# Performance work log

Measured on AMD Instinct MI355X. Metric: run time of the kernel, lower is better.

Reference implementation:

```python
import jax, jax.numpy as jnp
import numpy as np

IN_F, OUT_F, GS = 4096, 4096, 128
N_GROUPS = OUT_F * IN_F // GS  # 131072
TOKENS = 8192  # batch 4 * seq 2048


def setup_inputs() -> dict:
    key = jax.random.key(0)
    k1, k2, k3 = jax.random.split(key, 3)
    x = jax.random.normal(k1, (TOKENS, IN_F), dtype=jnp.float32)
    # ternary values in {-1, 0, 1}
    ternary = jax.random.randint(k2, (OUT_F, IN_F), -1, 2, dtype=jnp.int32).astype(jnp.int8)
    # per-group positive scales (beta), like abs-mean init, clamped > 0
    scales = jax.random.uniform(k3, (N_GROUPS,), dtype=jnp.float32, minval=0.01, maxval=0.1)
    ste_gain = jnp.ones((1,), dtype=jnp.float32)
    ste_temp = jnp.ones((1,), dtype=jnp.float32)
    return {"x": x, "ternary": ternary, "scales": scales,
            "ste_gain": ste_gain, "ste_temp": ste_temp}


def reference(x, ternary, scales, ste_gain, ste_temp):
    # Dequantize: each group of GS consecutive weights (row-major over [out,in])
    # shares one scale. scale_exp has shape [OUT_F, IN_F].
    scale_exp = jnp.repeat(scales, GS).reshape(OUT_F, IN_F)
    w = ternary.astype(jnp.float32) * scale_exp  # [out, in]
    # F.linear(x, w) = x @ w.T  (ste_gain/ste_temp affect only backward)
    return jnp.dot(x, w.T)
```

## Files before the change

kernel.cpp:

```cpp
#include <hip/hip_runtime.h>

#define TOKENS 8192
#define IN_F   4096
#define OUT_F  4096

#define BM 256
#define BN 256
#define BK 64
#define NT (IN_F / BK)

typedef __attribute__((ext_vector_type(4))) float  f32x4;
typedef __attribute__((ext_vector_type(4))) int    i32x4;

typedef const __attribute__((address_space(1))) void gas_void;
typedef __attribute__((address_space(3))) void las_void;

__global__ __launch_bounds__(256) void quant_x_kernel(const float* __restrict__ x,
                                                      signed char* __restrict__ xq,
                                                      float* __restrict__ dx) {
    const int row  = blockIdx.x;
    const int tid  = threadIdx.x;
    const int lane = tid & 63;
    const int wv   = tid >> 6;
    const float* xr = x + (size_t)row * IN_F;

    float v[16];
#pragma unroll
    for (int k = 0; k < 4; ++k) {
        f32x4 t = *(const f32x4*)(xr + k * 1024 + tid * 4);
#pragma unroll
        for (int j = 0; j < 4; ++j) v[k * 4 + j] = t[j];
    }
    float m = 0.f;
#pragma unroll
    for (int j = 0; j < 16; ++j) m = fmaxf(m, fabsf(v[j]));
#pragma unroll
    for (int off = 32; off >= 1; off >>= 1) m = fmaxf(m, __shfl_xor(m, off));
    __shared__ float sm[4];
    if (lane == 0) sm[wv] = m;
    __syncthreads();
    m = fmaxf(fmaxf(sm[0], sm[1]), fmaxf(sm[2], sm[3]));

    const float inv = 127.0f / m;
    if (tid == 0) dx[row] = m * (1.0f / 127.0f);

    int* out = (int*)(xq + (size_t)row * IN_F);
#pragma unroll
    for (int k = 0; k < 4; ++k) {
        int p = 0;
#pragma unroll
        for (int j = 0; j < 4; ++j) {
            int q = (int)rintf(v[k * 4 + j] * inv);
            p |= (q & 0xff) << (8 * j);
        }
        out[k * 256 + tid] = p;
    }
}

__global__ __launch_bounds__(256) void quant_w_kernel(const int* __restrict__ tern,
                                                      const float* __restrict__ scales,
                                                      signed char* __restrict__ wq,
                                                      float* __restrict__ dw) {
    const int o0   = blockIdx.x << 4;
    const int tid  = threadIdx.x;
    const int lane = tid & 63;
    const int lr   = lane & 15;
    const int lg   = lane >> 4;
    const int kt0  = tid >> 6;

    const int o = o0 + lr;
    const float* sr = scales + o * 32;
    float smax = 0.f;
#pragma unroll
    for (int g = 0; g < 32; ++g) smax = fmaxf(smax, sr[g]);
    const float rs = 127.0f / smax;
    if (tid < 16) dw[o0 + tid] = smax * (1.0f / 127.0f);

    const int bn  = o0 >> 8;
    const int g16 = (o0 >> 4) & 15;
    signed char* outb = wq + ((size_t)((bn * 64) * 16 + g16) << 10) + lane * 16;

#pragma unroll
    for (int i = 0; i < 16; ++i) {
        const int kt = kt0 * 16 + i;
        const int c  = kt * 4 + lg;
        const int iq = (int)rintf(sr[c >> 3] * rs);
        const i32x4* tp = (const i32x4*)(tern + (size_t)o * IN_F + c * 16);
        i32x4 w4;
#pragma unroll
        for (int k = 0; k < 4; ++k) {
            i32x4 tt = tp[k];
            int p = 0;
#pragma unroll
            for (int j = 0; j < 4; ++j) p |= ((tt[j] * iq) & 0xff) << (8 * j);
            w4[k] = p;
        }
        *(i32x4*)(outb + ((size_t)(kt * 16) << 10)) = w4;
    }
}


#define QUAD(MI0, NI0, BC)                                                     \
  do {                                                                         \
    __builtin_amdgcn_s_setprio(1);                                             \
    _Pragma("unroll") for (int mi = 0; mi < 4; ++mi)                           \
      _Pragma("unroll") for (int ni = 0; ni < 2; ++ni)                         \
          acc[(MI0)+mi][(NI0)+ni] = __builtin_amdgcn_mfma_i32_16x16x64_i8(     \
              a[(MI0)+mi], BC[(NI0)+ni], acc[(MI0)+mi][(NI0)+ni], 0, 0, 0);    \
    __builtin_amdgcn_s_setprio(0);                                             \
  } while (0)

#define BODY(T, BC, BNX)                                                       \
  do {                                                                         \
    const int abase_ = ((T) % 3) * 16384;                                      \
    _Pragma("unroll") for (int mi = 0; mi < 8; ++mi)                           \
        a[mi] = *(const i32x4*)&As[abase_ + pA[mi]];                           \
    if ((T) + 1 < NT) {                                                        \
      _Pragma("unroll") for (int ni = 0; ni < 4; ++ni)                         \
          BNX[ni] = *(const i32x4*)(bF + ni * 1024 + ((T) + 1) * 16384);       \
    }                                                                          \
    if ((T) + 2 < NT) stage_tile(((T) + 2) % 3, ((T) + 2) * BK);               \
    QUAD(0, 0, BC); QUAD(0, 2, BC); QUAD(4, 0, BC); QUAD(4, 2, BC);            \
    if ((T) + 2 < NT)      asm volatile("s_waitcnt vmcnt(6)" ::: "memory");    \
    else if ((T) + 1 < NT) asm volatile("s_waitcnt vmcnt(4)" ::: "memory");    \
    __builtin_amdgcn_sched_barrier(0);                                         \
    __builtin_amdgcn_s_barrier();                                              \
    __builtin_amdgcn_sched_barrier(0);                                         \
  } while (0)

__global__ __launch_bounds__(512, 2) void gemm_i8_kernel(
        const signed char* __restrict__ A,
        const signed char* __restrict__ B,
        const float* __restrict__ dX,
        const float* __restrict__ dW,
        float* __restrict__ C) {
    __shared__ __align__(16) signed char As[3 * 16384];

    const int tid  = threadIdx.x;
    const int wave = tid >> 6;
    const int lane = tid & 63;
    const int wm   = wave >> 2;
    const int wn   = wave & 3;
    const int lg   = lane >> 4;
    const int lr   = lane & 15;

    int bid = blockIdx.x;
    bid = (bid & 7) * (512 >> 3) + (bid >> 3);
    const int bm = bid >> 4;
    const int bn = bid & 15;

    const size_t a_row0 = (size_t)bm * BM;
    const size_t b_row0 = (size_t)bn * BN;

    const int sx  = (tid & 7) ^ ((tid >> 3) & 7);
    const int s_r = ((tid >> 3) << 1) | ((sx >> 2) & 1);
    const int s_c = (sx & 3) << 4;

    auto stage_half = [&](int buf, int h, int k0) {
        const signed char* src = A + (a_row0 + h * 128 + s_r) * IN_F + k0 + s_c;
        signed char* dst = As + buf * 16384 + h * 8192 + (wave << 10);
        __builtin_amdgcn_global_load_lds((gas_void*)src, (las_void*)dst, 16, 0, 0);
    };
    auto stage_tile = [&](int buf, int k0) { stage_half(buf, 0, k0); stage_half(buf, 1, k0); };

    i32x4 acc[8][4] = {};
    i32x4 a[8], bA[4], bB[4];

    auto physoff = [&](int r, int c0) {
        return ((r >> 1) << 7) + (((((r & 1) << 6) | c0) ^ (((r >> 1) & 7) << 4)));
    };
    int pA[8];
#pragma unroll
    for (int mi = 0; mi < 8; ++mi) pA[mi] = physoff(wm * 128 + mi * 16 + lr, lg << 4);

    const signed char* bF = B + ((size_t)(bn * 64 * 16 + wn * 4) << 10) + lane * 16;

    stage_tile(0, 0); stage_tile(1, BK);
#pragma unroll
    for (int ni = 0; ni < 4; ++ni) bA[ni] = *(const i32x4*)(bF + ni * 1024);
    asm volatile("s_waitcnt vmcnt(6)" ::: "memory");
    __builtin_amdgcn_sched_barrier(0);
    __builtin_amdgcn_s_barrier();
    __builtin_amdgcn_sched_barrier(0);

    for (int tt = 0; tt < NT; tt += 2) {
        BODY(tt,     bA, bB);
        BODY(tt + 1, bB, bA);
    }

    float dwc[4];
#pragma unroll
    for (int ni = 0; ni < 4; ++ni) dwc[ni] = dW[b_row0 + wn * 64 + ni * 16 + lr];

    float* Cp = C + (a_row0 + wm * 128) * (size_t)OUT_F + b_row0 + wn * 64;
#pragma unroll
    for (int mi = 0; mi < 8; ++mi) {
#pragma unroll
        for (int j = 0; j < 4; ++j) {
            const int r = mi * 16 + lg * 4 + j;
            const float dxr = dX[a_row0 + wm * 128 + r];
#pragma unroll
            for (int ni = 0; ni < 4; ++ni)
                Cp[(size_t)r * OUT_F + ni * 16 + lr] =
                    (float)acc[mi][ni][j] * dxr * dwc[ni];
        }
    }
}

extern "C" void kernel_launch(void* const* d_in, const int* in_sizes, int n_in,
                              void* d_out, int out_size, void* d_ws, size_t ws_size,
                              hipStream_t stream) {
    const float* x      = (const float*)d_in[0];
    const int*   tern   = (const int*)d_in[1];
    const float* scales = (const float*)d_in[2];

    signed char* xq = (signed char*)d_ws;
    signed char* wq = xq + (size_t)TOKENS * IN_F;
    float*       dx = (float*)(wq + (size_t)OUT_F * IN_F);
    float*       dw = dx + TOKENS;

    quant_x_kernel<<<TOKENS, 256, 0, stream>>>(x, xq, dx);
    quant_w_kernel<<<OUT_F / 16, 256, 0, stream>>>(tern, scales, wq, dw);

    dim3 grid((TOKENS / BM) * (OUT_F / BN));
    gemm_i8_kernel<<<grid, 512, 0, stream>>>(xq, wq, dx, dw, (float*)d_out);
}
```

Measured before the change: 203.5 us.

## Pre-swizzle activations into MFMA fragment layout and load both operands directly to registers

The activation quantize kernel now handles 16 rows per block and writes int8 activations in the same fragment-tiled layout used for weights. The GEMM drops the LDS staging and the barriers and loads A and B fragments straight from global memory into double-buffered registers, and the block-to-tile mapping changes. This removes LDS traffic and synchronisation, but each wave now fetches its own A fragments from global/L2 with no sharing, and load latency is hidden only by register double buffering.

```diff
diff --git a/kernel.cpp b/kernel.cpp
--- a/kernel.cpp
+++ b/kernel.cpp
@@ -12,48 +12,51 @@
 typedef __attribute__((ext_vector_type(4))) float  f32x4;
 typedef __attribute__((ext_vector_type(4))) int    i32x4;
 
-typedef const __attribute__((address_space(1))) void gas_void;
-typedef __attribute__((address_space(3))) void las_void;
+__global__ __launch_bounds__(256) void quant_x_kernel(const float* __restrict__ x,
+                                                      signed char* __restrict__ aq,
+                                                      float* __restrict__ dx) {
+    const int g   = blockIdx.x;
+    const int tid = threadIdx.x;
+    const float* xr0 = x + (size_t)g * 16 * IN_F;
 
-__global__ __launch_bounds__(256) void quant_x_kernel(const float* __restrict__ x,
-                                                      signed char* __restrict__ xq,
-                                                      float* __restrict__ dx) {
-    const int row  = blockIdx.x;
-    const int tid  = threadIdx.x;
-    const int lane = tid & 63;
-    const int wv   = tid >> 6;
-    const float* xr = x + (size_t)row * IN_F;
+    const int r1 = tid >> 4;
+    const int c1 = tid & 15;
+    float m = 0.f;
+    const float* p = xr0 + (size_t)r1 * IN_F + c1 * 4;
+    for (int s = 0; s < 64; ++s) {
+        f32x4 v = *(const f32x4*)(p + s * 64);
+        m = fmaxf(fmaxf(fabsf(v[0]), fabsf(v[1])),
+                  fmaxf(fmaxf(fabsf(v[2]), fabsf(v[3])), m));
+    }
+#pragma unroll
+    for (int off = 1; off < 16; off <<= 1) m = fmaxf(m, __shfl_xor(m, off));
+    __shared__ float sm[16];
+    if (c1 == 0) sm[r1] = m;
+    __syncthreads();
+    if (tid < 16) dx[g * 16 + tid] = sm[tid] * (1.0f / 127.0f);
 
-    float v[16];
+    const int lane = tid & 63, w = tid >> 6;
+    const int lr = lane & 15, cg = lane >> 4;
+    const float inv = 127.0f / sm[lr];
+    const float* xp = xr0 + (size_t)lr * IN_F;
+    signed char* outb = aq + (((size_t)(w * 16) * 512 + g) << 10) + lane * 16;
+
+    for (int s = 0; s < 16; ++s) {
+        const int kt = w * 16 + s;
+        const f32x4* src = (const f32x4*)(xp + kt * 64 + cg * 16);
+        i32x4 o;
 #pragma unroll
-    for (int k = 0; k < 4; ++k) {
-        f32x4 t = *(const f32x4*)(xr + k * 1024 + tid * 4);
+        for (int k = 0; k < 4; ++k) {
+            f32x4 v = src[k];
+            int pk = 0;
 #pragma unroll
-        for (int j = 0; j < 4; ++j) v[k * 4 + j] = t[j];
-    }
-    float m = 0.f;
-#pragma unroll
-    for (int j = 0; j < 16; ++j) m = fmaxf(m, fabsf(v[j]));
-#pragma unroll
-    for (int off = 32; off >= 1; off >>= 1) m = fmaxf(m, __shfl_xor(m, off));
-    __shared__ float sm[4];
-    if (lane == 0) sm[wv] = m;
-    __syncthreads();
-    m = fmaxf(fmaxf(sm[0], sm[1]), fmaxf(sm[2], sm[3]));
-
-    const float inv = 127.0f / m;
-    if (tid == 0) dx[row] = m * (1.0f / 127.0f);
-
-    int* out = (int*)(xq + (size_t)row * IN_F);
-#pragma unroll
-    for (int k = 0; k < 4; ++k) {
-        int p = 0;
-#pragma unroll
-        for (int j = 0; j < 4; ++j) {
-            int q = (int)rintf(v[k * 4 + j] * inv);
-            p |= (q & 0xff) << (8 * j);
+            for (int j = 0; j < 4; ++j) {
+                int q = (int)rintf(v[j] * inv);
+                pk |= (q & 0xff) << (8 * j);
+            }
+            o[k] = pk;
         }
-        out[k * 256 + tid] = p;
+        *(i32x4*)(outb + ((size_t)s * 512 << 10)) = o;
     }
 }
 
@@ -90,42 +93,32 @@
 #pragma unroll
         for (int k = 0; k < 4; ++k) {
             i32x4 tt = tp[k];
-            int p = 0;
+            int pk = 0;
 #pragma unroll
-            for (int j = 0; j < 4; ++j) p |= ((tt[j] * iq) & 0xff) << (8 * j);
-            w4[k] = p;
+            for (int j = 0; j < 4; ++j) pk |= ((tt[j] * iq) & 0xff) << (8 * j);
+            w4[k] = pk;
         }
         *(i32x4*)(outb + ((size_t)(kt * 16) << 10)) = w4;
     }
 }
 
 
-#define QUAD(MI0, NI0, BC)                                                     \
+#define MFMA_ALL(AF, BF)                                                       \
   do {                                                                         \
     __builtin_amdgcn_s_setprio(1);                                             \
-    _Pragma("unroll") for (int mi = 0; mi < 4; ++mi)                           \
-      _Pragma("unroll") for (int ni = 0; ni < 2; ++ni)                         \
-          acc[(MI0)+mi][(NI0)+ni] = __builtin_amdgcn_mfma_i32_16x16x64_i8(     \
-              a[(MI0)+mi], BC[(NI0)+ni], acc[(MI0)+mi][(NI0)+ni], 0, 0, 0);    \
+    _Pragma("unroll") for (int mi = 0; mi < 8; ++mi)                           \
+      _Pragma("unroll") for (int ni = 0; ni < 4; ++ni)                         \
+          acc[mi][ni] = __builtin_amdgcn_mfma_i32_16x16x64_i8(                 \
+              AF[mi], BF[ni], acc[mi][ni], 0, 0, 0);                           \
     __builtin_amdgcn_s_setprio(0);                                             \
   } while (0)
 
-#define BODY(T, BC, BNX)                                                       \
+#define LOADF(AF, BF, T)                                                       \
   do {                                                                         \
-    const int abase_ = ((T) % 3) * 16384;                                      \
     _Pragma("unroll") for (int mi = 0; mi < 8; ++mi)                           \
-        a[mi] = *(const i32x4*)&As[abase_ + pA[mi]];                           \
-    if ((T) + 1 < NT) {                                                        \
-      _Pragma("unroll") for (int ni = 0; ni < 4; ++ni)                         \
-          BNX[ni] = *(const i32x4*)(bF + ni * 1024 + ((T) + 1) * 16384);       \
-    }                                                                          \
-    if ((T) + 2 < NT) stage_tile(((T) + 2) % 3, ((T) + 2) * BK);               \
-    QUAD(0, 0, BC); QUAD(0, 2, BC); QUAD(4, 0, BC); QUAD(4, 2, BC);            \
-    if ((T) + 2 < NT)      asm volatile("s_waitcnt vmcnt(6)" ::: "memory");    \
-    else if ((T) + 1 < NT) asm volatile("s_waitcnt vmcnt(4)" ::: "memory");    \
-    __builtin_amdgcn_sched_barrier(0);                                         \
-    __builtin_amdgcn_s_barrier();                                              \
-    __builtin_amdgcn_sched_barrier(0);                                         \
+        AF[mi] = *(const i32x4*)(aB + (((size_t)(T) * 512 + mi) << 10));       \
+    _Pragma("unroll") for (int ni = 0; ni < 4; ++ni)                           \
+        BF[ni] = *(const i32x4*)(bB + (((size_t)(T) * 16 + ni) << 10));        \
   } while (0)
 
 __global__ __launch_bounds__(512, 2) void gemm_i8_kernel(
@@ -134,8 +127,6 @@
         const float* __restrict__ dX,
         const float* __restrict__ dW,
         float* __restrict__ C) {
-    __shared__ __align__(16) signed char As[3 * 16384];
-
     const int tid  = threadIdx.x;
     const int wave = tid >> 6;
     const int lane = tid & 63;
@@ -144,48 +135,28 @@
     const int lg   = lane >> 4;
     const int lr   = lane & 15;
 
-    int bid = blockIdx.x;
-    bid = (bid & 7) * (512 >> 3) + (bid >> 3);
-    const int bm = bid >> 4;
-    const int bn = bid & 15;
+    const int bid = blockIdx.x;
+    const int bn  = ((bid & 7) << 1) | (bid >> 8);
+    const int bm  = (bid >> 3) & 31;
 
     const size_t a_row0 = (size_t)bm * BM;
     const size_t b_row0 = (size_t)bn * BN;
 
-    const int sx  = (tid & 7) ^ ((tid >> 3) & 7);
-    const int s_r = ((tid >> 3) << 1) | ((sx >> 2) & 1);
-    const int s_c = (sx & 3) << 4;
-
-    auto stage_half = [&](int buf, int h, int k0) {
-        const signed char* src = A + (a_row0 + h * 128 + s_r) * IN_F + k0 + s_c;
-        signed char* dst = As + buf * 16384 + h * 8192 + (wave << 10);
-        __builtin_amdgcn_global_load_lds((gas_void*)src, (las_void*)dst, 16, 0, 0);
-    };
-    auto stage_tile = [&](int buf, int k0) { stage_half(buf, 0, k0); stage_half(buf, 1, k0); };
+    const signed char* aB = A + (((size_t)(bm * 16 + wm * 8)) << 10) + lane * 16;
+    const signed char* bB = B + (((size_t)(bn * 64 * 16 + wn * 4)) << 10) + lane * 16;
 
     i32x4 acc[8][4] = {};
-    i32x4 a[8], bA[4], bB[4];
+    i32x4 aX[8], bX[4], aY[8], bY[4];
 
-    auto physoff = [&](int r, int c0) {
-        return ((r >> 1) << 7) + (((((r & 1) << 6) | c0) ^ (((r >> 1) & 7) << 4)));
-    };
-    int pA[8];
-#pragma unroll
-    for (int mi = 0; mi < 8; ++mi) pA[mi] = physoff(wm * 128 + mi * 16 + lr, lg << 4);
+    LOADF(aX, bX, 0);
+    LOADF(aY, bY, 1);
 
-    const signed char* bF = B + ((size_t)(bn * 64 * 16 + wn * 4) << 10) + lane * 16;
-
-    stage_tile(0, 0); stage_tile(1, BK);
-#pragma unroll
-    for (int ni = 0; ni < 4; ++ni) bA[ni] = *(const i32x4*)(bF + ni * 1024);
-    asm volatile("s_waitcnt vmcnt(6)" ::: "memory");
-    __builtin_amdgcn_sched_barrier(0);
-    __builtin_amdgcn_s_barrier();
-    __builtin_amdgcn_sched_barrier(0);
-
-    for (int tt = 0; tt < NT; tt += 2) {
-        BODY(tt,     bA, bB);
-        BODY(tt + 1, bB, bA);
+    for (int i = 0; i < NT / 2; ++i) {
+        const int t0 = 2 * i;
+        MFMA_ALL(aX, bX);
+        if (t0 + 2 < NT) LOADF(aX, bX, t0 + 2);
+        MFMA_ALL(aY, bY);
+        if (t0 + 3 < NT) LOADF(aY, bY, t0 + 3);
     }
 
     float dwc[4];
@@ -219,7 +190,7 @@
     float*       dx = (float*)(wq + (size_t)OUT_F * IN_F);
     float*       dw = dx + TOKENS;
 
-    quant_x_kernel<<<TOKENS, 256, 0, stream>>>(x, xq, dx);
+    quant_x_kernel<<<TOKENS / 16, 256, 0, stream>>>(x, xq, dx);
     quant_w_kernel<<<OUT_F / 16, 256, 0, stream>>>(tern, scales, wq, dw);
 
     dim3 grid((TOKENS / BM) * (OUT_F / BN));
```

New measurement: 220.0 us. 1.08x slower.

## Reorder GEMM prefetch ahead of LDS reads and simplify barriers and block mapping

Applied to the files above, without the earlier changes.

Each GEMM iteration now issues the next B register load and the A tile stage for step T+2 before reading A fragments from LDS. A scheduling barrier fences those loads off, and the hand-tuned vmcnt waits plus raw s_barrier are replaced with a plain __syncthreads. The block-index swizzle is also changed to a different mapping from blockIdx to (bm, bn) tiles. The aim is to issue memory traffic earlier, but __syncthreads likely drains all outstanding global loads each step, shrinking the effective prefetch depth and possibly exposing load latency.

```diff
diff --git a/kernel.cpp b/kernel.cpp
--- a/kernel.cpp
+++ b/kernel.cpp
@@ -90,10 +90,10 @@
 #pragma unroll
         for (int k = 0; k < 4; ++k) {
             i32x4 tt = tp[k];
-            int p = 0;
-#pragma unroll
-            for (int j = 0; j < 4; ++j) p |= ((tt[j] * iq) & 0xff) << (8 * j);
-            w4[k] = p;
+            int pk = 0;
+#pragma unroll
+            for (int j = 0; j < 4; ++j) pk |= ((tt[j] * iq) & 0xff) << (8 * j);
+            w4[k] = pk;
         }
         *(i32x4*)(outb + ((size_t)(kt * 16) << 10)) = w4;
     }
@@ -110,22 +110,22 @@
     __builtin_amdgcn_s_setprio(0);                                             \
   } while (0)
 
+#define LOADB(BF, T)                                                           \
+  do {                                                                         \
+    _Pragma("unroll") for (int ni = 0; ni < 4; ++ni)                           \
+        BF[ni] = *(const i32x4*)(bF + (ni << 10) + ((size_t)(T) << 14));       \
+  } while (0)
+
 #define BODY(T, BC, BNX)                                                       \
   do {                                                                         \
+    if ((T) + 1 < NT) LOADB(BNX, (T) + 1);                                     \
+    if ((T) + 2 < NT) stage_tile(((T) + 2) % 3, ((T) + 2) * BK);               \
+    __builtin_amdgcn_sched_barrier(0);               \
     const int abase_ = ((T) % 3) * 16384;                                      \
     _Pragma("unroll") for (int mi = 0; mi < 8; ++mi)                           \
         a[mi] = *(const i32x4*)&As[abase_ + pA[mi]];                           \
-    if ((T) + 1 < NT) {                                                        \
-      _Pragma("unroll") for (int ni = 0; ni < 4; ++ni)                         \
-          BNX[ni] = *(const i32x4*)(bF + ni * 1024 + ((T) + 1) * 16384);       \
-    }                                                                          \
-    if ((T) + 2 < NT) stage_tile(((T) + 2) % 3, ((T) + 2) * BK);               \
     QUAD(0, 0, BC); QUAD(0, 2, BC); QUAD(4, 0, BC); QUAD(4, 2, BC);            \
-    if ((T) + 2 < NT)      asm volatile("s_waitcnt vmcnt(6)" ::: "memory");    \
-    else if ((T) + 1 < NT) asm volatile("s_waitcnt vmcnt(4)" ::: "memory");    \
-    __builtin_amdgcn_sched_barrier(0);                                         \
-    __builtin_amdgcn_s_barrier();                                              \
-    __builtin_amdgcn_sched_barrier(0);                                         \
+    __syncthreads();                                                           \
   } while (0)
 
 __global__ __launch_bounds__(512, 2) void gemm_i8_kernel(
@@ -144,10 +144,9 @@
     const int lg   = lane >> 4;
     const int lr   = lane & 15;
 
-    int bid = blockIdx.x;
-    bid = (bid & 7) * (512 >> 3) + (bid >> 3);
-    const int bm = bid >> 4;
-    const int bn = bid & 15;
+    const int bid = blockIdx.x;
+    const int bn  = ((bid & 7) << 1) | (bid >> 8);
+    const int bm  = (bid >> 3) & 31;
 
     const size_t a_row0 = (size_t)bm * BM;
     const size_t b_row0 = (size_t)bn * BN;
@@ -173,15 +172,11 @@
 #pragma unroll
     for (int mi = 0; mi < 8; ++mi) pA[mi] = physoff(wm * 128 + mi * 16 + lr, lg << 4);
 
-    const signed char* bF = B + ((size_t)(bn * 64 * 16 + wn * 4) << 10) + lane * 16;
+    const signed char* bF = B + (((size_t)(bn * 64 * 16 + wn * 4)) << 10) + lane * 16;
 
     stage_tile(0, 0); stage_tile(1, BK);
-#pragma unroll
-    for (int ni = 0; ni < 4; ++ni) bA[ni] = *(const i32x4*)(bF + ni * 1024);
-    asm volatile("s_waitcnt vmcnt(6)" ::: "memory");
-    __builtin_amdgcn_sched_barrier(0);
-    __builtin_amdgcn_s_barrier();
-    __builtin_amdgcn_sched_barrier(0);
+    LOADB(bA, 0);
+    __syncthreads();
 
     for (int tt = 0; tt < NT; tt += 2) {
         BODY(tt,     bA, bB);
```

After: 223.7 us. +9.9%, slower.
